# Kernel tuning notes

Measured on AMD Instinct MI355X. Metric: run time of the kernel, lower is better.

The kernel has to match this reference:

```python
import jax, jax.numpy as jnp
import numpy as np

B, L, H, E = 2, 2048, 16, 64
BLOCK_SIZE = 256


def setup_inputs() -> dict:
    key = jax.random.key(0)
    kq, kk, kv = jax.random.split(key, 3)
    return {
        "queries": jax.random.normal(kq, (B, L, H, E), dtype=jnp.float32),
        "keys": jax.random.normal(kk, (B, L, H, E), dtype=jnp.float32),
        "values": jax.random.normal(kv, (B, L, H, E), dtype=jnp.float32),
        "block_size": BLOCK_SIZE,
    }


def reference(queries, keys, values, block_size):
    # Faithful to the torch module: NO 1/sqrt(E) scaling is applied.
    Bq, Lq, Hq, Eq = queries.shape
    # dense scores [B, H, L, S]
    scores = jnp.einsum("blhe,bshe->bhls", queries, keys)
    # block-diagonal mask: positions in the same block of size block_size
    idx = jnp.arange(Lq)
    block_mask = (idx[:, None] // block_size) == (idx[None, :] // block_size)  # [L, L]
    neg_inf = jnp.asarray(-jnp.inf, dtype=scores.dtype)
    scores = jnp.where(block_mask[None, None, :, :], scores, neg_inf)
    attn = jax.nn.softmax(scores, axis=-1)  # each row has its diagonal block unmasked
    output = jnp.einsum("bhls,bshd->blhd", attn, values)
    return (output, attn)
```

## Files before the change

### kernel.cpp

```cpp
#include <hip/hip_runtime.h>

#define Bq   2
#define Lq   2048
#define Hq   16
#define Eq   64
#define BSq  256
#define SUB  64


__global__ __launch_bounds__(256, 1)
void sparse_attn(const float* __restrict__ qp,
                 const float* __restrict__ kp,
                 const float* __restrict__ vp,
                 float* __restrict__ outp)
{
    extern __shared__ float smem[];
    float (*S)[257] = (float (*)[257])smem;
    float4* KV      = (float4*)(smem + 64*257);
    float*  mred    = smem + 64*257 + 4096*4;
    float*  lred    = mred + 256;
    float*  invl    = lred + 256;

    const int w   = blockIdx.x;
    const int sub = w & 3;
    const int qb  = (w >> 2) & 7;
    const int h   = (w >> 5) & 15;
    const int b   = w >> 9;
    const int R0  = qb * BSq + sub * SUB;

    const int t    = threadIdx.x;
    const int r    = t & 63;
    const int part = t >> 6;

    float* attn = outp + (size_t)Bq * Lq * Hq * Eq;

    const float* kbase = kp + (((size_t)b * Lq + qb * BSq) * Hq + h) * Eq;
    #pragma unroll
    for (int i = 0; i < 16; ++i) {
        int idx = i * 256 + t;
        int s   = idx >> 4;
        int e4  = idx & 15;
        KV[idx] = *(const float4*)(kbase + (size_t)s * (Hq * Eq) + e4 * 4);
    }
    const float* qrow = qp + (((size_t)b * Lq + R0 + r) * Hq + h) * Eq;
    float4 qreg[16];
    #pragma unroll
    for (int j = 0; j < 16; ++j) qreg[j] = *(const float4*)(qrow + 4 * j);
    __syncthreads();

    float lmax = -3.4e38f;
    #pragma unroll 2
    for (int sl = 0; sl < 64; ++sl) {
        int s = part * 64 + sl;
        float p0 = 0.f, p1 = 0.f, p2 = 0.f, p3 = 0.f;
        #pragma unroll
        for (int j = 0; j < 16; ++j) {
            float4 kv = KV[s * 16 + j];
            p0 = fmaf(qreg[j].x, kv.x, p0);
            p1 = fmaf(qreg[j].y, kv.y, p1);
            p2 = fmaf(qreg[j].z, kv.z, p2);
            p3 = fmaf(qreg[j].w, kv.w, p3);
        }
        float sc = (p0 + p1) + (p2 + p3);
        S[r][s] = sc;
        lmax = fmaxf(lmax, sc);
    }
    mred[part * 64 + r] = lmax;
    __syncthreads();

    const float* vbase = vp + (((size_t)b * Lq + qb * BSq) * Hq + h) * Eq;
    #pragma unroll
    for (int i = 0; i < 16; ++i) {
        int idx = i * 256 + t;
        int s   = idx >> 4;
        int e4  = idx & 15;
        KV[idx] = *(const float4*)(vbase + (size_t)s * (Hq * Eq) + e4 * 4);
    }
    float m = fmaxf(fmaxf(mred[r], mred[64 + r]), fmaxf(mred[128 + r], mred[192 + r]));
    float lsum = 0.f;
    #pragma unroll 2
    for (int sl = 0; sl < 64; ++sl) {
        int s = part * 64 + sl;
        float e = __expf(S[r][s] - m);
        S[r][s] = e;
        lsum += e;
    }
    lred[part * 64 + r] = lsum;
    __syncthreads();
    const float linv = 1.0f / (lred[r] + lred[64 + r] + lred[128 + r] + lred[192 + r]);
    if (part == 0) invl[r] = linv;

    float4 acc[16];
    #pragma unroll
    for (int j = 0; j < 16; ++j) acc[j] = make_float4(0.f, 0.f, 0.f, 0.f);
    #pragma unroll 2
    for (int sl = 0; sl < 64; ++sl) {
        int s = part * 64 + sl;
        float p = S[r][s];
        #pragma unroll
        for (int j = 0; j < 16; ++j) {
            float4 vv = KV[s * 16 + j];
            acc[j].x = fmaf(p, vv.x, acc[j].x);
            acc[j].y = fmaf(p, vv.y, acc[j].y);
            acc[j].z = fmaf(p, vv.z, acc[j].z);
            acc[j].w = fmaf(p, vv.w, acc[j].w);
        }
    }
    __syncthreads();

    float* red = (float*)KV;
    if (part != 0) {
        float* dst = red + (size_t)(part - 1) * 4160 + r * 65;
        #pragma unroll
        for (int j = 0; j < 16; ++j) {
            dst[4 * j + 0] = acc[j].x;
            dst[4 * j + 1] = acc[j].y;
            dst[4 * j + 2] = acc[j].z;
            dst[4 * j + 3] = acc[j].w;
        }
    }
    __syncthreads();
    if (part == 0) {
        float* orow = outp + (((size_t)b * Lq + R0 + r) * Hq + h) * Eq;
        const float* s0 = red + r * 65;
        const float* s1 = red + 4160 + r * 65;
        const float* s2 = red + 8320 + r * 65;
        #pragma unroll
        for (int j = 0; j < 16; ++j) {
            float4 val = acc[j];
            val.x = (val.x + s0[4 * j + 0] + s1[4 * j + 0] + s2[4 * j + 0]) * linv;
            val.y = (val.y + s0[4 * j + 1] + s1[4 * j + 1] + s2[4 * j + 1]) * linv;
            val.z = (val.z + s0[4 * j + 2] + s1[4 * j + 2] + s2[4 * j + 2]) * linv;
            val.w = (val.w + s0[4 * j + 3] + s1[4 * j + 3] + s2[4 * j + 3]) * linv;
            *(float4*)(orow + 4 * j) = val;
        }
    }

    float* ablock = attn + (((size_t)b * Hq + h) * Lq + R0) * Lq;
    #pragma unroll 2
    for (int i = 0; i < 64; ++i) {
        ablock[(size_t)i * Lq + qb * BSq + t] = S[i][t] * invl[i];
    }
    float4* abase4 = (float4*)ablock;
    const int qb64 = qb * 64;
    const float4 z = make_float4(0.f, 0.f, 0.f, 0.f);
    #pragma unroll 2
    for (int i = 0; i < 112; ++i) {
        int f   = i * 256 + t;
        int row = f / 448;
        int j   = f - row * 448;
        int c4  = (j < qb64) ? j : j + 64;
        abase4[(size_t)row * 512 + c4] = z;
    }
}

extern "C" void kernel_launch(void* const* d_in, const int* in_sizes, int n_in,
                              void* d_out, int out_size, void* d_ws, size_t ws_size,
                              hipStream_t stream) {
    const float* q = (const float*)d_in[0];
    const float* k = (const float*)d_in[1];
    const float* v = (const float*)d_in[2];
    float* out = (float*)d_out;

    const size_t lds_bytes = (64 * 257 + 4096 * 4 + 256 + 256 + 64) * sizeof(float);
    (void)hipFuncSetAttribute((const void*)sparse_attn,
                              hipFuncAttributeMaxDynamicSharedMemorySize,
                              (int)lds_bytes);

    dim3 grid(Bq * Hq * 8 * 4);
    dim3 block(256);
    hipLaunchKernelGGL(sparse_attn, grid, block, lds_bytes, stream, q, k, v, out);
}
```

Measured before the change: 797.5 us.

## Register-tile QK and PV, store probabilities as bf16, interleave zero-fill

Rewrites the kernel to compute QK^T with an 8x8 register tile per thread over staged Q/K chunks, and PV with a 4-row tile over swizzled V chunks. Normalized probabilities are kept in LDS as bf16, which shrinks LDS so two blocks fit per CU. The zero-fill of the masked attention matrix is split into chunks interleaved with the compute phases to overlap stores with math. The bf16 rounding of the attention weights lowers precision of both outputs and may exceed the tolerance.

Result: faster. 754.4 us (-5.4%).

```diff
diff --git a/kernel.cpp b/kernel.cpp
--- a/kernel.cpp
+++ b/kernel.cpp
@@ -1,157 +1,240 @@
 #include <hip/hip_runtime.h>
 
-#define Bq   2
-#define Lq   2048
-#define Hq   16
-#define Eq   64
-#define BSq  256
-#define SUB  64
-
-
-__global__ __launch_bounds__(256, 1)
-void sparse_attn(const float* __restrict__ qp,
-                 const float* __restrict__ kp,
-                 const float* __restrict__ vp,
-                 float* __restrict__ outp)
-{
-    extern __shared__ float smem[];
-    float (*S)[257] = (float (*)[257])smem;
-    float4* KV      = (float4*)(smem + 64*257);
-    float*  mred    = smem + 64*257 + 4096*4;
-    float*  lred    = mred + 256;
-    float*  invl    = lred + 256;
-
-    const int w   = blockIdx.x;
-    const int sub = w & 3;
-    const int qb  = (w >> 2) & 7;
-    const int h   = (w >> 5) & 15;
-    const int b   = w >> 9;
-    const int R0  = qb * BSq + sub * SUB;
-
-    const int t    = threadIdx.x;
-    const int r    = t & 63;
-    const int part = t >> 6;
-
-    float* attn = outp + (size_t)Bq * Lq * Hq * Eq;
-
-    const float* kbase = kp + (((size_t)b * Lq + qb * BSq) * Hq + h) * Eq;
-    #pragma unroll
-    for (int i = 0; i < 16; ++i) {
-        int idx = i * 256 + t;
-        int s   = idx >> 4;
-        int e4  = idx & 15;
-        KV[idx] = *(const float4*)(kbase + (size_t)s * (Hq * Eq) + e4 * 4);
-    }
-    const float* qrow = qp + (((size_t)b * Lq + R0 + r) * Hq + h) * Eq;
-    float4 qreg[16];
-    #pragma unroll
-    for (int j = 0; j < 16; ++j) qreg[j] = *(const float4*)(qrow + 4 * j);
-    __syncthreads();
-
-    float lmax = -3.4e38f;
-    #pragma unroll 2
-    for (int sl = 0; sl < 64; ++sl) {
-        int s = part * 64 + sl;
-        float p0 = 0.f, p1 = 0.f, p2 = 0.f, p3 = 0.f;
-        #pragma unroll
-        for (int j = 0; j < 16; ++j) {
-            float4 kv = KV[s * 16 + j];
-            p0 = fmaf(qreg[j].x, kv.x, p0);
-            p1 = fmaf(qreg[j].y, kv.y, p1);
-            p2 = fmaf(qreg[j].z, kv.z, p2);
-            p3 = fmaf(qreg[j].w, kv.w, p3);
-        }
-        float sc = (p0 + p1) + (p2 + p3);
-        S[r][s] = sc;
-        lmax = fmaxf(lmax, sc);
-    }
-    mred[part * 64 + r] = lmax;
-    __syncthreads();
-
-    const float* vbase = vp + (((size_t)b * Lq + qb * BSq) * Hq + h) * Eq;
-    #pragma unroll
-    for (int i = 0; i < 16; ++i) {
-        int idx = i * 256 + t;
-        int s   = idx >> 4;
-        int e4  = idx & 15;
-        KV[idx] = *(const float4*)(vbase + (size_t)s * (Hq * Eq) + e4 * 4);
-    }
-    float m = fmaxf(fmaxf(mred[r], mred[64 + r]), fmaxf(mred[128 + r], mred[192 + r]));
-    float lsum = 0.f;
-    #pragma unroll 2
-    for (int sl = 0; sl < 64; ++sl) {
-        int s = part * 64 + sl;
-        float e = __expf(S[r][s] - m);
-        S[r][s] = e;
-        lsum += e;
-    }
-    lred[part * 64 + r] = lsum;
-    __syncthreads();
-    const float linv = 1.0f / (lred[r] + lred[64 + r] + lred[128 + r] + lred[192 + r]);
-    if (part == 0) invl[r] = linv;
-
-    float4 acc[16];
-    #pragma unroll
-    for (int j = 0; j < 16; ++j) acc[j] = make_float4(0.f, 0.f, 0.f, 0.f);
-    #pragma unroll 2
-    for (int sl = 0; sl < 64; ++sl) {
-        int s = part * 64 + sl;
-        float p = S[r][s];
-        #pragma unroll
-        for (int j = 0; j < 16; ++j) {
-            float4 vv = KV[s * 16 + j];
-            acc[j].x = fmaf(p, vv.x, acc[j].x);
-            acc[j].y = fmaf(p, vv.y, acc[j].y);
-            acc[j].z = fmaf(p, vv.z, acc[j].z);
-            acc[j].w = fmaf(p, vv.w, acc[j].w);
-        }
-    }
-    __syncthreads();
-
-    float* red = (float*)KV;
-    if (part != 0) {
-        float* dst = red + (size_t)(part - 1) * 4160 + r * 65;
-        #pragma unroll
-        for (int j = 0; j < 16; ++j) {
-            dst[4 * j + 0] = acc[j].x;
-            dst[4 * j + 1] = acc[j].y;
-            dst[4 * j + 2] = acc[j].z;
-            dst[4 * j + 3] = acc[j].w;
-        }
-    }
-    __syncthreads();
-    if (part == 0) {
-        float* orow = outp + (((size_t)b * Lq + R0 + r) * Hq + h) * Eq;
-        const float* s0 = red + r * 65;
-        const float* s1 = red + 4160 + r * 65;
-        const float* s2 = red + 8320 + r * 65;
-        #pragma unroll
-        for (int j = 0; j < 16; ++j) {
-            float4 val = acc[j];
-            val.x = (val.x + s0[4 * j + 0] + s1[4 * j + 0] + s2[4 * j + 0]) * linv;
-            val.y = (val.y + s0[4 * j + 1] + s1[4 * j + 1] + s2[4 * j + 1]) * linv;
-            val.z = (val.z + s0[4 * j + 2] + s1[4 * j + 2] + s2[4 * j + 2]) * linv;
-            val.w = (val.w + s0[4 * j + 3] + s1[4 * j + 3] + s2[4 * j + 3]) * linv;
-            *(float4*)(orow + 4 * j) = val;
-        }
-    }
-
-    float* ablock = attn + (((size_t)b * Hq + h) * Lq + R0) * Lq;
-    #pragma unroll 2
-    for (int i = 0; i < 64; ++i) {
-        ablock[(size_t)i * Lq + qb * BSq + t] = S[i][t] * invl[i];
-    }
-    float4* abase4 = (float4*)ablock;
-    const int qb64 = qb * 64;
+#define Bq 2
+#define Lq 2048
+#define Hq 16
+#define Eq 64
+#define HE (Hq * Eq)
+
+#define QS_STRIDE 68
+#define KV_OFF    4352
+#define RED_OFF   9472
+#define SP_OFF    9984
+#define SP_STRIDE 272
+
+__device__ __forceinline__ unsigned short f2bf(float x) {
+    unsigned u = __float_as_uint(x);
+    return (unsigned short)((u + 0x7fffu + ((u >> 16) & 1u)) >> 16);
+}
+__device__ __forceinline__ float bf2f(unsigned short s) {
+    return __uint_as_float(((unsigned)s) << 16);
+}
+
+__device__ __forceinline__ void fill_chunk(float4* __restrict__ abase4, int qb64, int t, int c) {
     const float4 z = make_float4(0.f, 0.f, 0.f, 0.f);
-    #pragma unroll 2
-    for (int i = 0; i < 112; ++i) {
-        int f   = i * 256 + t;
+    #pragma unroll
+    for (int i = 0; i < 14; ++i) {
+        int f   = (c * 14 + i) * 256 + t;
         int row = f / 448;
         int j   = f - row * 448;
         int c4  = (j < qb64) ? j : j + 64;
         abase4[(size_t)row * 512 + c4] = z;
     }
+}
+
+__global__ __launch_bounds__(256, 2)
+void sparse_attn(const float* __restrict__ qp, const float* __restrict__ kp,
+                 const float* __restrict__ vp, float* __restrict__ outp)
+{
+    extern __shared__ float smem[];
+    float* Qs  = smem;
+    float* KVs = smem + KV_OFF;
+    float* red = smem + RED_OFF;
+    unsigned short* Sp = (unsigned short*)(smem + SP_OFF);
+
+    const int w3  = blockIdx.x;
+    const int sub = w3 & 3, qb = (w3 >> 2) & 7, h = (w3 >> 5) & 15, b = w3 >> 9;
+    const int R0  = qb * 256 + sub * 64;
+
+    const int t = threadIdx.x;
+    const int wv = t >> 6, lane = t & 63, rg = lane & 7, cg = lane >> 3;
+
+    const float* qbase = qp + ((size_t)(b * Lq + R0) * Hq + h) * Eq;
+    const float* kbase = kp + ((size_t)(b * Lq + qb * 256) * Hq + h) * Eq;
+    const float* vbase = vp + ((size_t)(b * Lq + qb * 256) * Hq + h) * Eq;
+    float* attn   = outp + (size_t)Bq * Lq * Hq * Eq;
+    float* ablock = attn + ((size_t)(b * Hq + h) * Lq + R0) * Lq;
+    float4* abase4 = (float4*)ablock;
+    const int qb64 = qb * 64;
+
+    #pragma unroll
+    for (int i = 0; i < 4; ++i) {
+        int idx = i * 256 + t, row = idx >> 4, e4 = idx & 15;
+        *(float4*)&Qs[row * QS_STRIDE + e4 * 4] =
+            *(const float4*)(qbase + (size_t)row * HE + e4 * 4);
+    }
+    #pragma unroll
+    for (int i = 0; i < 4; ++i) {
+        int idx = i * 256 + t, key = idx >> 2, e4 = idx & 3;
+        *(float4*)&KVs[key * 20 + e4 * 4] =
+            *(const float4*)(kbase + (size_t)key * HE + e4 * 4);
+    }
+    __syncthreads();
+
+    float sc[8][8];
+    #pragma unroll
+    for (int i = 0; i < 8; ++i)
+        #pragma unroll
+        for (int j = 0; j < 8; ++j) sc[i][j] = 0.f;
+
+    for (int rd = 0; rd < 4; ++rd) {
+        #pragma unroll
+        for (int kc = 0; kc < 4; ++kc) {
+            float4 qf[8], kf[8];
+            #pragma unroll
+            for (int i = 0; i < 8; ++i)
+                qf[i] = *(float4*)&Qs[(rg + 8 * i) * QS_STRIDE + rd * 16 + kc * 4];
+            #pragma unroll
+            for (int j = 0; j < 8; ++j)
+                kf[j] = *(float4*)&KVs[(wv * 64 + cg + 8 * j) * 20 + kc * 4];
+            #pragma unroll
+            for (int i = 0; i < 8; ++i)
+                #pragma unroll
+                for (int j = 0; j < 8; ++j)
+                    sc[i][j] = fmaf(qf[i].x, kf[j].x,
+                               fmaf(qf[i].y, kf[j].y,
+                               fmaf(qf[i].z, kf[j].z,
+                               fmaf(qf[i].w, kf[j].w, sc[i][j]))));
+        }
+        if (rd < 3) {
+            __syncthreads();
+            #pragma unroll
+            for (int i = 0; i < 4; ++i) {
+                int idx = i * 256 + t, key = idx >> 2, e4 = idx & 3;
+                *(float4*)&KVs[key * 20 + e4 * 4] =
+                    *(const float4*)(kbase + (size_t)key * HE + (rd + 1) * 16 + e4 * 4);
+            }
+            fill_chunk(abase4, qb64, t, rd);
+            __syncthreads();
+        }
+    }
+
+    float mrow[8];
+    #pragma unroll
+    for (int i = 0; i < 8; ++i) {
+        float m = sc[i][0];
+        #pragma unroll
+        for (int j = 1; j < 8; ++j) m = fmaxf(m, sc[i][j]);
+        m = fmaxf(m, __shfl_xor(m, 8));
+        m = fmaxf(m, __shfl_xor(m, 16));
+        m = fmaxf(m, __shfl_xor(m, 32));
+        mrow[i] = m;
+    }
+    if (cg == 0) {
+        #pragma unroll
+        for (int i = 0; i < 8; ++i) red[wv * 64 + rg + 8 * i] = mrow[i];
+    }
+    __syncthreads();
+
+    #pragma unroll
+    for (int i = 0; i < 4; ++i) {
+        int idx = i * 256 + t, k63 = idx >> 4, e4 = idx & 15;
+        *(float4*)&KVs[(k63 * 16 + (e4 ^ (k63 >> 3))) * 4] =
+            *(const float4*)(vbase + (size_t)k63 * HE + e4 * 4);
+    }
+
+    float lrow[8];
+    #pragma unroll
+    for (int i = 0; i < 8; ++i) {
+        int r = rg + 8 * i;
+        float m = fmaxf(fmaxf(red[r], red[64 + r]), fmaxf(red[128 + r], red[192 + r]));
+        float l = 0.f;
+        #pragma unroll
+        for (int j = 0; j < 8; ++j) {
+            float e = __expf(sc[i][j] - m);
+            sc[i][j] = e;
+            l += e;
+        }
+        l += __shfl_xor(l, 8);
+        l += __shfl_xor(l, 16);
+        l += __shfl_xor(l, 32);
+        lrow[i] = l;
+    }
+    if (cg == 0) {
+        #pragma unroll
+        for (int i = 0; i < 8; ++i) red[256 + wv * 64 + rg + 8 * i] = lrow[i];
+    }
+    __syncthreads();
+
+    #pragma unroll
+    for (int i = 0; i < 8; ++i) {
+        int r = rg + 8 * i;
+        float linv = 1.0f / (red[256 + r] + red[320 + r] + red[384 + r] + red[448 + r]);
+        unsigned u0 = (unsigned)f2bf(sc[i][0] * linv) | ((unsigned)f2bf(sc[i][1] * linv) << 16);
+        unsigned u1 = (unsigned)f2bf(sc[i][2] * linv) | ((unsigned)f2bf(sc[i][3] * linv) << 16);
+        unsigned u2 = (unsigned)f2bf(sc[i][4] * linv) | ((unsigned)f2bf(sc[i][5] * linv) << 16);
+        unsigned u3 = (unsigned)f2bf(sc[i][6] * linv) | ((unsigned)f2bf(sc[i][7] * linv) << 16);
+        *(uint4*)&Sp[r * SP_STRIDE + wv * 64 + cg * 8] = make_uint4(u0, u1, u2, u3);
+    }
+    fill_chunk(abase4, qb64, t, 3);
+    __syncthreads();
+
+    const int r4 = lane & 3, d4 = lane >> 2;
+    float4 acc[4];
+    #pragma unroll
+    for (int i = 0; i < 4; ++i) acc[i] = make_float4(0.f, 0.f, 0.f, 0.f);
+
+    for (int kb = 0; kb < 4; ++kb) {
+        if (kb) {
+            __syncthreads();
+            #pragma unroll
+            for (int i = 0; i < 4; ++i) {
+                int idx = i * 256 + t, k63 = idx >> 4, e4 = idx & 15;
+                *(float4*)&KVs[(k63 * 16 + (e4 ^ (k63 >> 3))) * 4] =
+                    *(const float4*)(vbase + (size_t)(kb * 64 + k63) * HE + e4 * 4);
+            }
+            fill_chunk(abase4, qb64, t, 3 + kb);
+            __syncthreads();
+        }
+        #pragma unroll
+        for (int c = 0; c < 8; ++c) {
+            float pv[4][8];
+            #pragma unroll
+            for (int i = 0; i < 4; ++i) {
+                int row = 16 * wv + r4 + 4 * i;
+                uint4 pw = *(uint4*)&Sp[row * SP_STRIDE + kb * 64 + c * 8];
+                pv[i][0] = __uint_as_float(pw.x << 16);
+                pv[i][1] = __uint_as_float(pw.x & 0xffff0000u);
+                pv[i][2] = __uint_as_float(pw.y << 16);
+                pv[i][3] = __uint_as_float(pw.y & 0xffff0000u);
+                pv[i][4] = __uint_as_float(pw.z << 16);
+                pv[i][5] = __uint_as_float(pw.z & 0xffff0000u);
+                pv[i][6] = __uint_as_float(pw.w << 16);
+                pv[i][7] = __uint_as_float(pw.w & 0xffff0000u);
+            }
+            #pragma unroll
+            for (int k = 0; k < 8; ++k) {
+                float4 vv = *(float4*)&KVs[((c + 8 * k) * 16 + (d4 ^ k)) * 4];
+                #pragma unroll
+                for (int i = 0; i < 4; ++i) {
+                    acc[i].x = fmaf(pv[i][k], vv.x, acc[i].x);
+                    acc[i].y = fmaf(pv[i][k], vv.y, acc[i].y);
+                    acc[i].z = fmaf(pv[i][k], vv.z, acc[i].z);
+                    acc[i].w = fmaf(pv[i][k], vv.w, acc[i].w);
+                }
+            }
+        }
+    }
+
+    #pragma unroll
+    for (int i = 0; i < 4; ++i) {
+        int row = 16 * wv + r4 + 4 * i;
+        *(float4*)(outp + ((size_t)(b * Lq + R0 + row) * Hq + h) * Eq + d4 * 4) = acc[i];
+    }
+
+    #pragma unroll 4
+    for (int i = 0; i < 16; ++i) {
+        int idx = i * 256 + t, row = idx >> 6, c4 = idx & 63, c = c4 * 4;
+        int basep = row * SP_STRIDE + (c & 0xC0) + ((c >> 3) & 7);
+        int c7 = c & 7;
+        float4 v;
+        v.x = bf2f(Sp[basep + (c7 + 0) * 8]);
+        v.y = bf2f(Sp[basep + (c7 + 1) * 8]);
+        v.z = bf2f(Sp[basep + (c7 + 2) * 8]);
+        v.w = bf2f(Sp[basep + (c7 + 3) * 8]);
+        *(float4*)(ablock + (size_t)row * Lq + qb * 256 + c) = v;
+    }
+    fill_chunk(abase4, qb64, t, 7);
 }
 
 extern "C" void kernel_launch(void* const* d_in, const int* in_sizes, int n_in,
@@ -162,7 +245,7 @@
     const float* v = (const float*)d_in[2];
     float* out = (float*)d_out;
 
-    const size_t lds_bytes = (64 * 257 + 4096 * 4 + 256 + 256 + 64) * sizeof(float);
+    const size_t lds_bytes = SP_OFF * sizeof(float) + 64 * SP_STRIDE * sizeof(unsigned short);
     (void)hipFuncSetAttribute((const void*)sparse_attn,
                               hipFuncAttributeMaxDynamicSharedMemorySize,
                               (int)lds_bytes);
```
